# Optimization experiments

Measured on AMD Instinct MI355X. Metric: run time of the kernel, lower is better.

## Reference

```python
import jax, jax.numpy as jnp
from jax import lax
import numpy as np

NUM_BINS = 4
GROUPS = 196
PS = 16  # patch_size
CH = 3 * GROUPS  # 588


def quick_gelu(x):
    return x * jax.nn.sigmoid(1.702 * x)


def avgpool3_exclude_pad(x):
    # AvgPool2d(kernel=3, stride=1, padding=1, count_include_pad=False)
    win = (1, 1, 3, 3)
    strides = (1, 1, 1, 1)
    pad = ((0, 0), (0, 0), (1, 1), (1, 1))
    s = lax.reduce_window(x, jnp.float32(0.0), lax.add, win, strides, pad)
    ones = jnp.ones((1, 1) + x.shape[-2:], x.dtype)
    cnt = lax.reduce_window(ones, jnp.float32(0.0), lax.add, win, strides, pad)
    return s / cnt


def setup_inputs() -> dict:
    key = jax.random.key(0)
    ks = jax.random.split(key, 6)
    B = 64
    x = jax.random.normal(ks[0], (B, 197, 768), jnp.float32)
    # adapter_conv: Conv2d(588,588,3,groups=196) -> OIHW weight [588,3,3,3]
    conv_w = jax.random.normal(ks[1], (CH, 3, 3, 3), jnp.float32) * (1.0 / np.sqrt(27.0))
    conv_b = jnp.zeros((CH,), jnp.float32)
    # HistogramLayer: bin_centers_conv.bias (learnable), bin_widths_conv.weight (learnable)
    centers = jax.random.normal(ks[2], (NUM_BINS * CH,), jnp.float32) * 0.1
    widths = jax.random.normal(ks[3], (NUM_BINS * CH,), jnp.float32) * 0.1 + 1.0
    # adapter_conv_down: Conv2d(2352,588,1,groups=196) -> per-group [3 out, 12 in]
    down_w = jax.random.normal(ks[4], (GROUPS, 3, 12), jnp.float32) * 0.1
    down_b = jax.random.normal(ks[5], (CH,), jnp.float32) * 0.1
    return dict(x=x, conv_w=conv_w, conv_b=conv_b, centers=centers,
                widths=widths, down_w=down_w, down_b=down_b)


def reference(x, conv_w, conv_b, centers, widths, down_w, down_b):
    B, N, C = x.shape  # (64, 197, 768)
    x_cls = x[:, :1, :]
    xp = x[:, 1:, :].reshape(B, (N - 1) * 3, PS, PS)  # (B, 588, 16, 16)

    # grouped 3x3 conv, groups=196 (3->3 per group)
    y = lax.conv_general_dilated(
        xp, conv_w, window_strides=(1, 1), padding=((1, 1), (1, 1)),
        dimension_numbers=('NCHW', 'OIHW', 'NCHW'), feature_group_count=GROUPS)
    y = y + conv_b[None, :, None, None]
    y = quick_gelu(y)

    # HistogramLayer: bin_centers (weight frozen at 1) -> abs; bin_widths (bias frozen at 1) -> relu
    h = jnp.abs(jnp.repeat(y, NUM_BINS, axis=1) + centers[None, :, None, None])  # (B, 2352, 16, 16)
    h = jax.nn.relu(widths[None, :, None, None] * h + 1.0)

    # constrain_bins: per-(channel-group of 4 bins) sum-normalize
    Bn, Cn, H, W = h.shape
    hr = h.reshape(Bn, Cn // NUM_BINS, NUM_BINS, H, W)
    h = (hr / (hr.sum(axis=2, keepdims=True) + 1e-5)).reshape(Bn, Cn, H, W)

    # normalize_count: AvgPool2d(3, stride=1, pad=1, count_include_pad=False)
    h = avgpool3_exclude_pad(h)
    h = quick_gelu(h)

    # adapter_conv_down: grouped 1x1 conv, 12 -> 3 per group of 196
    hg = h.reshape(B, GROUPS, 12, H, W)
    o = jnp.einsum('bgihw,goi->bgohw', hg, down_w) + down_b.reshape(1, GROUPS, 3, 1, 1)
    o = o.reshape(B, GROUPS, 768)  # (3*16*16 = 768 per patch token)

    return jnp.concatenate([x_cls, o], axis=1)  # (B, 197, 768)
```

## Files before the change

kernel.cpp:

```cpp
#include <hip/hip_runtime.h>

#define GROUPS 196

__device__ __forceinline__ float dppL(float v) {
    return __int_as_float(__builtin_amdgcn_update_dpp(
        __float_as_int(v), __float_as_int(v), 0x111, 0xF, 0xF, true));
}
__device__ __forceinline__ float dppR(float v) {
    return __int_as_float(__builtin_amdgcn_update_dpp(
        __float_as_int(v), __float_as_int(v), 0x101, 0xF, 0xF, true));
}

__device__ __forceinline__ float qgelu(float v) {
    return v * __builtin_amdgcn_rcpf(1.0f + __expf(-1.702f * v));
}

__device__ __forceinline__ float qgelu01(float p) {
    float s = fmaf(p, 0.041056f, -0.126448f);
    s = fmaf(p, s, 0.006306f);
    s = fmaf(p, s, 0.424881f);
    s = fmaf(p, s, 0.5f);
    return p * s;
}

__global__ __launch_bounds__(256) void convpass_fused(
    const float* __restrict__ x,
    const float* __restrict__ conv_w,
    const float* __restrict__ conv_b,
    const float* __restrict__ centers,
    const float* __restrict__ widths,
    const float* __restrict__ down_w,
    const float* __restrict__ down_b,
    float* __restrict__ out)
{
    const int g = blockIdx.x;
    const int b = blockIdx.y;
    const int tid = threadIdx.x;
    const int px = tid & 15;
    const int py = tid >> 4;
    const int ip = (py + 1) * 16 + px;

    __shared__ float4 s_in[288];
    __shared__ float4 s_rs[3][288];

    if (tid < 32) {
        const int pix = (tid < 16) ? tid : (272 + (tid - 16));
        const float4 z = make_float4(0.f, 0.f, 0.f, 0.f);
        s_in[pix] = z;
        s_rs[0][pix] = z; s_rs[1][pix] = z; s_rs[2][pix] = z;
    }

    const float* xin = x + ((size_t)b * 197 + (size_t)(g + 1)) * 768;
    s_in[ip] = make_float4(xin[tid], xin[256 + tid], xin[512 + tid], 0.f);

    __syncthreads();

    const float* cw = conv_w + g * 81;
    float yy0 = conv_b[g * 3 + 0];
    float yy1 = conv_b[g * 3 + 1];
    float yy2 = conv_b[g * 3 + 2];

    const int vb = py * 16 + px;
    float4 vrow[3];
    vrow[0] = s_in[vb];
    vrow[1] = s_in[vb + 16];
    vrow[2] = s_in[vb + 32];

    #pragma unroll
    for (int ky = 0; ky < 3; ++ky) {
        const float c0 = vrow[ky].x, c1 = vrow[ky].y, c2 = vrow[ky].z;
        const float l0 = dppL(c0), l1 = dppL(c1), l2 = dppL(c2);
        const float r0 = dppR(c0), r1 = dppR(c1), r2 = dppR(c2);
        const float* w0 = cw + ky * 3;
        const float* w1 = cw + 27 + ky * 3;
        const float* w2 = cw + 54 + ky * 3;
        yy0 = fmaf(l0,w0[0],fmaf(c0,w0[1],fmaf(r0,w0[2],
              fmaf(l1,w0[9],fmaf(c1,w0[10],fmaf(r1,w0[11],
              fmaf(l2,w0[18],fmaf(c2,w0[19],fmaf(r2,w0[20], yy0)))))))));
        yy1 = fmaf(l0,w1[0],fmaf(c0,w1[1],fmaf(r0,w1[2],
              fmaf(l1,w1[9],fmaf(c1,w1[10],fmaf(r1,w1[11],
              fmaf(l2,w1[18],fmaf(c2,w1[19],fmaf(r2,w1[20], yy1)))))))));
        yy2 = fmaf(l0,w2[0],fmaf(c0,w2[1],fmaf(r0,w2[2],
              fmaf(l1,w2[9],fmaf(c1,w2[10],fmaf(r1,w2[11],
              fmaf(l2,w2[18],fmaf(c2,w2[19],fmaf(r2,w2[20], yy2)))))))));
    }

    const float* cen = centers + g * 12;
    const float* wid = widths  + g * 12;
    const float yv[3] = { qgelu(yy0), qgelu(yy1), qgelu(yy2) };
    float rs[12];
    #pragma unroll
    for (int oc = 0; oc < 3; ++oc) {
        const float t0 = fmaf(wid[oc*4+0], fabsf(yv[oc] + cen[oc*4+0]), 1.0f);
        const float t1 = fmaf(wid[oc*4+1], fabsf(yv[oc] + cen[oc*4+1]), 1.0f);
        const float t2 = fmaf(wid[oc*4+2], fabsf(yv[oc] + cen[oc*4+2]), 1.0f);
        const float t3 = fmaf(wid[oc*4+3], fabsf(yv[oc] + cen[oc*4+3]), 1.0f);
        const float inv = __builtin_amdgcn_rcpf((t0 + t1) + (t2 + t3));
        const float h0 = t0 * inv, h1 = t1 * inv, h2 = t2 * inv, h3 = t3 * inv;
        rs[oc*4+0] = h0 + dppL(h0) + dppR(h0);
        rs[oc*4+1] = h1 + dppL(h1) + dppR(h1);
        rs[oc*4+2] = h2 + dppL(h2) + dppR(h2);
        rs[oc*4+3] = h3 + dppL(h3) + dppR(h3);
        s_rs[oc][ip] = make_float4(rs[oc*4+0], rs[oc*4+1], rs[oc*4+2], rs[oc*4+3]);
    }

    __syncthreads();

    const float vx = (float)(1 + (px > 0) + (px < 15));
    const float vy = (float)(1 + (py > 0) + (py < 15));
    const float rcnt = __builtin_amdgcn_rcpf(vx * vy);

    const float* dwp = down_w + g * 36;
    float o0 = down_b[g * 3 + 0];
    float o1 = down_b[g * 3 + 1];
    float o2 = down_b[g * 3 + 2];

    #pragma unroll
    for (int oc = 0; oc < 3; ++oc) {
        const float4 up = s_rs[oc][ip - 16];
        const float4 dn = s_rs[oc][ip + 16];
        const float p0 = qgelu01((rs[oc*4+0] + up.x + dn.x) * rcnt);
        const float p1 = qgelu01((rs[oc*4+1] + up.y + dn.y) * rcnt);
        const float p2 = qgelu01((rs[oc*4+2] + up.z + dn.z) * rcnt);
        const float p3 = qgelu01((rs[oc*4+3] + up.w + dn.w) * rcnt);
        const int i = oc * 4;
        o0 = fmaf(p0,dwp[i],   fmaf(p1,dwp[i+1],   fmaf(p2,dwp[i+2],   fmaf(p3,dwp[i+3],   o0))));
        o1 = fmaf(p0,dwp[12+i],fmaf(p1,dwp[12+i+1],fmaf(p2,dwp[12+i+2],fmaf(p3,dwp[12+i+3],o1))));
        o2 = fmaf(p0,dwp[24+i],fmaf(p1,dwp[24+i+1],fmaf(p2,dwp[24+i+2],fmaf(p3,dwp[24+i+3],o2))));
    }

    float* outp = out + ((size_t)b * 197 + (size_t)(g + 1)) * 768;
    outp[tid]       = o0;
    outp[256 + tid] = o1;
    outp[512 + tid] = o2;

    if (g == 0) {
        const float* xc = x + (size_t)b * 197 * 768;
        float* op = out + (size_t)b * 197 * 768;
        op[tid]       = xc[tid];
        op[256 + tid] = xc[256 + tid];
        op[512 + tid] = xc[512 + tid];
    }
}

extern "C" void kernel_launch(void* const* d_in, const int* in_sizes, int n_in,
                              void* d_out, int out_size, void* d_ws, size_t ws_size,
                              hipStream_t stream) {
    const float* x       = (const float*)d_in[0];
    const float* conv_w  = (const float*)d_in[1];
    const float* conv_b  = (const float*)d_in[2];
    const float* centers = (const float*)d_in[3];
    const float* widths  = (const float*)d_in[4];
    const float* down_w  = (const float*)d_in[5];
    const float* down_b  = (const float*)d_in[6];
    float* out = (float*)d_out;

    const int B = in_sizes[0] / (197 * 768);

    dim3 grid(GROUPS, B);
    convpass_fused<<<grid, 256, 0, stream>>>(x, conv_w, conv_b, centers, widths,
                                             down_w, down_b, out);
}
```

Before: 36.23 us.

## Assign one group per wavefront with 4 pixels per lane and wave-local LDS

```diff
diff --git a/kernel.cpp b/kernel.cpp
--- a/kernel.cpp
+++ b/kernel.cpp
@@ -10,11 +10,9 @@
     return __int_as_float(__builtin_amdgcn_update_dpp(
         __float_as_int(v), __float_as_int(v), 0x101, 0xF, 0xF, true));
 }
-
 __device__ __forceinline__ float qgelu(float v) {
     return v * __builtin_amdgcn_rcpf(1.0f + __expf(-1.702f * v));
 }
-
 __device__ __forceinline__ float qgelu01(float p) {
     float s = fmaf(p, 0.041056f, -0.126448f);
     s = fmaf(p, s, 0.006306f);
@@ -22,6 +20,9 @@
     s = fmaf(p, s, 0.5f);
     return p * s;
 }
+
+#define LDS_FENCE() asm volatile("s_waitcnt lgkmcnt(0)" ::: "memory")
+#define F4C(v, j) ((j) == 0 ? (v).x : (j) == 1 ? (v).y : (j) == 2 ? (v).z : (v).w)
 
 __global__ __launch_bounds__(256) void convpass_fused(
     const float* __restrict__ x,
@@ -33,113 +34,170 @@
     const float* __restrict__ down_b,
     float* __restrict__ out)
 {
-    const int g = blockIdx.x;
-    const int b = blockIdx.y;
     const int tid = threadIdx.x;
-    const int px = tid & 15;
-    const int py = tid >> 4;
-    const int ip = (py + 1) * 16 + px;
-
-    __shared__ float4 s_in[288];
-    __shared__ float4 s_rs[3][288];
-
-    if (tid < 32) {
-        const int pix = (tid < 16) ? tid : (272 + (tid - 16));
+    const int l  = tid & 63;
+    const int wv = tid >> 6;
+    const int g  = blockIdx.x * 4 + wv;
+    const int b  = blockIdx.y;
+    const int py = l >> 2;
+    const int q  = l & 3;
+    const bool q0 = (q == 0), q3 = (q == 3);
+    const float mL = q0 ? 0.f : 1.f;
+    const float mR = q3 ? 0.f : 1.f;
+
+    __shared__ float4 sIN[4][3][18][4];
+    __shared__ float4 sRS[4][3][18][4];
+
+    const int sg = __builtin_amdgcn_readfirstlane(g);
+    const float* cw  = conv_w  + sg * 81;
+    const float* cen = centers + sg * 12;
+    const float* wid = widths  + sg * 12;
+    const float* dwp = down_w  + sg * 36;
+    const float cb0 = conv_b[sg*3+0], cb1 = conv_b[sg*3+1], cb2 = conv_b[sg*3+2];
+    const float db0 = down_b[sg*3+0], db1 = down_b[sg*3+1], db2 = down_b[sg*3+2];
+
+    const int tok = b * 197 + g + 1;
+    const float4* xin4 = (const float4*)x + tok * 192;
+    const float4 A0 = xin4[l];
+    const float4 A1 = xin4[64 + l];
+    const float4 A2 = xin4[128 + l];
+
+    if (l < 24) {
+        const int ic = l >> 3, rem = l & 7;
+        const int row = (rem >> 2) ? 17 : 0;
+        const int col = rem & 3;
         const float4 z = make_float4(0.f, 0.f, 0.f, 0.f);
-        s_in[pix] = z;
-        s_rs[0][pix] = z; s_rs[1][pix] = z; s_rs[2][pix] = z;
-    }
-
-    const float* xin = x + ((size_t)b * 197 + (size_t)(g + 1)) * 768;
-    s_in[ip] = make_float4(xin[tid], xin[256 + tid], xin[512 + tid], 0.f);
-
-    __syncthreads();
-
-    const float* cw = conv_w + g * 81;
-    float yy0 = conv_b[g * 3 + 0];
-    float yy1 = conv_b[g * 3 + 1];
-    float yy2 = conv_b[g * 3 + 2];
-
-    const int vb = py * 16 + px;
-    float4 vrow[3];
-    vrow[0] = s_in[vb];
-    vrow[1] = s_in[vb + 16];
-    vrow[2] = s_in[vb + 32];
-
-    #pragma unroll
-    for (int ky = 0; ky < 3; ++ky) {
-        const float c0 = vrow[ky].x, c1 = vrow[ky].y, c2 = vrow[ky].z;
-        const float l0 = dppL(c0), l1 = dppL(c1), l2 = dppL(c2);
-        const float r0 = dppR(c0), r1 = dppR(c1), r2 = dppR(c2);
-        const float* w0 = cw + ky * 3;
-        const float* w1 = cw + 27 + ky * 3;
-        const float* w2 = cw + 54 + ky * 3;
-        yy0 = fmaf(l0,w0[0],fmaf(c0,w0[1],fmaf(r0,w0[2],
-              fmaf(l1,w0[9],fmaf(c1,w0[10],fmaf(r1,w0[11],
-              fmaf(l2,w0[18],fmaf(c2,w0[19],fmaf(r2,w0[20], yy0)))))))));
-        yy1 = fmaf(l0,w1[0],fmaf(c0,w1[1],fmaf(r0,w1[2],
-              fmaf(l1,w1[9],fmaf(c1,w1[10],fmaf(r1,w1[11],
-              fmaf(l2,w1[18],fmaf(c2,w1[19],fmaf(r2,w1[20], yy1)))))))));
-        yy2 = fmaf(l0,w2[0],fmaf(c0,w2[1],fmaf(r0,w2[2],
-              fmaf(l1,w2[9],fmaf(c1,w2[10],fmaf(r1,w2[11],
-              fmaf(l2,w2[18],fmaf(c2,w2[19],fmaf(r2,w2[20], yy2)))))))));
-    }
-
-    const float* cen = centers + g * 12;
-    const float* wid = widths  + g * 12;
-    const float yv[3] = { qgelu(yy0), qgelu(yy1), qgelu(yy2) };
-    float rs[12];
+        sIN[wv][ic][row][col] = z;
+        sRS[wv][ic][row][col] = z;
+    }
+    sIN[wv][0][py + 1][q] = A0;
+    sIN[wv][1][py + 1][q] = A1;
+    sIN[wv][2][py + 1][q] = A2;
+
+    LDS_FENCE();
+
+    float4 V[3][3];
+    V[0][1] = A0; V[1][1] = A1; V[2][1] = A2;
+    #pragma unroll
+    for (int ic = 0; ic < 3; ++ic) {
+        V[ic][0] = sIN[wv][ic][py][q];
+        V[ic][2] = sIN[wv][ic][py + 2][q];
+    }
+
+    float L[3][3], R[3][3];
+    #pragma unroll
+    for (int ic = 0; ic < 3; ++ic) {
+        #pragma unroll
+        for (int r = 0; r < 3; ++r) {
+            L[ic][r] = dppL(V[ic][r].w) * mL;
+            R[ic][r] = dppR(V[ic][r].x) * mR;
+        }
+    }
+
+    float acc[3][4];
+    #pragma unroll
+    for (int j = 0; j < 4; ++j) { acc[0][j] = cb0; acc[1][j] = cb1; acc[2][j] = cb2; }
     #pragma unroll
     for (int oc = 0; oc < 3; ++oc) {
-        const float t0 = fmaf(wid[oc*4+0], fabsf(yv[oc] + cen[oc*4+0]), 1.0f);
-        const float t1 = fmaf(wid[oc*4+1], fabsf(yv[oc] + cen[oc*4+1]), 1.0f);
-        const float t2 = fmaf(wid[oc*4+2], fabsf(yv[oc] + cen[oc*4+2]), 1.0f);
-        const float t3 = fmaf(wid[oc*4+3], fabsf(yv[oc] + cen[oc*4+3]), 1.0f);
-        const float inv = __builtin_amdgcn_rcpf((t0 + t1) + (t2 + t3));
-        const float h0 = t0 * inv, h1 = t1 * inv, h2 = t2 * inv, h3 = t3 * inv;
-        rs[oc*4+0] = h0 + dppL(h0) + dppR(h0);
-        rs[oc*4+1] = h1 + dppL(h1) + dppR(h1);
-        rs[oc*4+2] = h2 + dppL(h2) + dppR(h2);
-        rs[oc*4+3] = h3 + dppL(h3) + dppR(h3);
-        s_rs[oc][ip] = make_float4(rs[oc*4+0], rs[oc*4+1], rs[oc*4+2], rs[oc*4+3]);
-    }
-
-    __syncthreads();
-
-    const float vx = (float)(1 + (px > 0) + (px < 15));
-    const float vy = (float)(1 + (py > 0) + (py < 15));
-    const float rcnt = __builtin_amdgcn_rcpf(vx * vy);
-
-    const float* dwp = down_w + g * 36;
-    float o0 = down_b[g * 3 + 0];
-    float o1 = down_b[g * 3 + 1];
-    float o2 = down_b[g * 3 + 2];
+        #pragma unroll
+        for (int ic = 0; ic < 3; ++ic) {
+            #pragma unroll
+            for (int r = 0; r < 3; ++r) {
+                const float w0 = cw[oc*27 + ic*9 + r*3 + 0];
+                const float w1 = cw[oc*27 + ic*9 + r*3 + 1];
+                const float w2 = cw[oc*27 + ic*9 + r*3 + 2];
+                const float4 v = V[ic][r];
+                acc[oc][0] = fmaf(L[ic][r], w0, fmaf(v.x, w1, fmaf(v.y, w2, acc[oc][0])));
+                acc[oc][1] = fmaf(v.x,      w0, fmaf(v.y, w1, fmaf(v.z, w2, acc[oc][1])));
+                acc[oc][2] = fmaf(v.y,      w0, fmaf(v.z, w1, fmaf(v.w, w2, acc[oc][2])));
+                acc[oc][3] = fmaf(v.z,      w0, fmaf(v.w, w1, fmaf(R[ic][r], w2, acc[oc][3])));
+            }
+        }
+    }
+
+    float yv[3][4];
+    #pragma unroll
+    for (int oc = 0; oc < 3; ++oc)
+        #pragma unroll
+        for (int j = 0; j < 4; ++j)
+            yv[oc][j] = qgelu(acc[oc][j]);
+
+    const bool  vy2 = (py == 0) | (py == 15);
+    const float rEdge = vy2 ? 0.25f     : (1.f/6.f);
+    const float rMid  = vy2 ? (1.f/6.f) : (1.f/9.f);
+    const float rc[4] = { q0 ? rEdge : rMid, rMid, rMid, q3 ? rEdge : rMid };
+
+    float o[3][4];
+    #pragma unroll
+    for (int j = 0; j < 4; ++j) { o[0][j] = db0; o[1][j] = db1; o[2][j] = db2; }
 
     #pragma unroll
     for (int oc = 0; oc < 3; ++oc) {
-        const float4 up = s_rs[oc][ip - 16];
-        const float4 dn = s_rs[oc][ip + 16];
-        const float p0 = qgelu01((rs[oc*4+0] + up.x + dn.x) * rcnt);
-        const float p1 = qgelu01((rs[oc*4+1] + up.y + dn.y) * rcnt);
-        const float p2 = qgelu01((rs[oc*4+2] + up.z + dn.z) * rcnt);
-        const float p3 = qgelu01((rs[oc*4+3] + up.w + dn.w) * rcnt);
-        const int i = oc * 4;
-        o0 = fmaf(p0,dwp[i],   fmaf(p1,dwp[i+1],   fmaf(p2,dwp[i+2],   fmaf(p3,dwp[i+3],   o0))));
-        o1 = fmaf(p0,dwp[12+i],fmaf(p1,dwp[12+i+1],fmaf(p2,dwp[12+i+2],fmaf(p3,dwp[12+i+3],o1))));
-        o2 = fmaf(p0,dwp[24+i],fmaf(p1,dwp[24+i+1],fmaf(p2,dwp[24+i+2],fmaf(p3,dwp[24+i+3],o2))));
-    }
-
-    float* outp = out + ((size_t)b * 197 + (size_t)(g + 1)) * 768;
-    outp[tid]       = o0;
-    outp[256 + tid] = o1;
-    outp[512 + tid] = o2;
+        float hj[3][4];
+        #pragma unroll
+        for (int j = 0; j < 4; ++j) {
+            const float y = yv[oc][j];
+            const float t0 = fmaf(wid[oc*4+0], fabsf(y + cen[oc*4+0]), 1.0f);
+            const float t1 = fmaf(wid[oc*4+1], fabsf(y + cen[oc*4+1]), 1.0f);
+            const float t2 = fmaf(wid[oc*4+2], fabsf(y + cen[oc*4+2]), 1.0f);
+            const float t3 = fmaf(wid[oc*4+3], fabsf(y + cen[oc*4+3]), 1.0f);
+            const float inv = __builtin_amdgcn_rcpf((t0 + t1) + (t2 + t3));
+            hj[0][j] = t0 * inv; hj[1][j] = t1 * inv; hj[2][j] = t2 * inv;
+        }
+        float rs[3][4];
+        #pragma unroll
+        for (int k = 0; k < 3; ++k) {
+            const float lh = dppL(hj[k][3]) * mL;
+            const float rh = dppR(hj[k][0]) * mR;
+            const float s01 = hj[k][0] + hj[k][1];
+            const float s23 = hj[k][2] + hj[k][3];
+            rs[k][0] = lh + s01;
+            rs[k][1] = s01 + hj[k][2];
+            rs[k][2] = hj[k][1] + s23;
+            rs[k][3] = s23 + rh;
+        }
+
+        LDS_FENCE();
+        #pragma unroll
+        for (int k = 0; k < 3; ++k)
+            sRS[wv][k][py + 1][q] = make_float4(rs[k][0], rs[k][1], rs[k][2], rs[k][3]);
+        LDS_FENCE();
+
+        float4 up[3], dn[3];
+        #pragma unroll
+        for (int k = 0; k < 3; ++k) {
+            up[k] = sRS[wv][k][py][q];
+            dn[k] = sRS[wv][k][py + 2][q];
+        }
+
+        #pragma unroll
+        for (int j = 0; j < 4; ++j) {
+            const float p0 = (rs[0][j] + F4C(up[0], j) + F4C(dn[0], j)) * rc[j];
+            const float p1 = (rs[1][j] + F4C(up[1], j) + F4C(dn[1], j)) * rc[j];
+            const float p2 = (rs[2][j] + F4C(up[2], j) + F4C(dn[2], j)) * rc[j];
+            const float p3 = 1.0f - p0 - p1 - p2;
+            const float u0 = qgelu01(p0);
+            const float u1 = qgelu01(p1);
+            const float u2 = qgelu01(p2);
+            const float u3 = qgelu01(p3);
+            const int i = oc * 4;
+            o[0][j] = fmaf(u0, dwp[i],    fmaf(u1, dwp[i+1],    fmaf(u2, dwp[i+2],    fmaf(u3, dwp[i+3],    o[0][j]))));
+            o[1][j] = fmaf(u0, dwp[12+i], fmaf(u1, dwp[12+i+1], fmaf(u2, dwp[12+i+2], fmaf(u3, dwp[12+i+3], o[1][j]))));
+            o[2][j] = fmaf(u0, dwp[24+i], fmaf(u1, dwp[24+i+1], fmaf(u2, dwp[24+i+2], fmaf(u3, dwp[24+i+3], o[2][j]))));
+        }
+    }
+
+    float4* op4 = (float4*)out + tok * 192;
+    op4[l]       = make_float4(o[0][0], o[0][1], o[0][2], o[0][3]);
+    op4[64 + l]  = make_float4(o[1][0], o[1][1], o[1][2], o[1][3]);
+    op4[128 + l] = make_float4(o[2][0], o[2][1], o[2][2], o[2][3]);
 
     if (g == 0) {
-        const float* xc = x + (size_t)b * 197 * 768;
-        float* op = out + (size_t)b * 197 * 768;
-        op[tid]       = xc[tid];
-        op[256 + tid] = xc[256 + tid];
-        op[512 + tid] = xc[512 + tid];
+        const float4* xc = (const float4*)x + b * 197 * 192;
+        float4* oc4 = (float4*)out + b * 197 * 192;
+        oc4[l]       = xc[l];
+        oc4[64 + l]  = xc[64 + l];
+        oc4[128 + l] = xc[128 + l];
     }
 }
 
@@ -157,7 +215,7 @@
 
     const int B = in_sizes[0] / (197 * 768);
 
-    dim3 grid(GROUPS, B);
+    dim3 grid(GROUPS / 4, B);
     convpass_fused<<<grid, 256, 0, stream>>>(x, conv_w, conv_b, centers, widths,
                                              down_w, down_b, out);
 }
```

New measurement: 30.60 us. -15.5%, faster.
